# Kernel tuning notes

Hardware: AMD Instinct MI355X
Metric: run time of the kernel (lower is better)

The kernel has to match this reference:

```python
import jax, jax.numpy as jnp
import numpy as np

B, M, D, H = 2, 2048, 1024, 16
DH = D // H            # 64 head dim
FF = 2624              # GeGLU intermediate size
EPS = 1e-5
ROPE_BASE = 10000.0


def _layernorm(x, g, b):
    mu = jnp.mean(x, axis=-1, keepdims=True)
    var = jnp.mean(jnp.square(x - mu), axis=-1, keepdims=True)
    return (x - mu) * jax.lax.rsqrt(var + EPS) * g + b


def _rope_cos_sin(m, dh):
    # HF-style: inv_freq over even dims; only first dh/2 entries are used by apply_rope
    inv_freq = 1.0 / (ROPE_BASE ** (jnp.arange(0, dh, 2, dtype=jnp.float32) / dh))  # [dh/2]
    ang = jnp.arange(m, dtype=jnp.float32)[:, None] * inv_freq[None, :]             # [M, dh/2]
    return jnp.cos(ang), jnp.sin(ang)


def _apply_rope(x, c, s):
    # x: [B,H,M,dh]; c,s: [M,dh/2] broadcast over B,H. Half-split (non-interleaved) rotation.
    x1, x2 = jnp.split(x, 2, axis=-1)
    return jnp.concatenate([x1 * c - x2 * s, x1 * s + x2 * c], axis=-1)


def setup_inputs() -> dict:
    key = jax.random.key(0)
    ks = jax.random.split(key, 6)
    w = lambda k, shape: (jax.random.normal(k, shape, jnp.float32) * 0.02)
    return {
        "hidden_states": jax.random.normal(ks[0], (B, M, D), jnp.float32),
        "attention_mask": jnp.ones((B, M), jnp.int32),
        "ln1_g": jnp.ones((D,), jnp.float32),
        "ln1_b": jnp.zeros((D,), jnp.float32),
        "Wqkv_w": w(ks[1], (3 * D, D)),
        "Wqkv_b": jnp.zeros((3 * D,), jnp.float32),
        "Wo_w": w(ks[2], (D, D)),
        "ln2_g": jnp.ones((D,), jnp.float32),
        "ln2_b": jnp.zeros((D,), jnp.float32),
        "Wi_w": w(ks[3], (2 * FF, D)),
        "Wmlp_o_w": w(ks[4], (D, FF)),
    }


def reference(hidden_states, attention_mask, ln1_g, ln1_b, Wqkv_w, Wqkv_b, Wo_w,
              ln2_g, ln2_b, Wi_w, Wmlp_o_w):
    x = hidden_states                                    # [B,M,D]
    xn = _layernorm(x, ln1_g, ln1_b)
    qkv = xn @ Wqkv_w.T + Wqkv_b                         # [B,M,3D]
    qkv = qkv.reshape(B, M, 3, H, DH).transpose(0, 3, 1, 2, 4)  # [B,H,M,3,dh]
    q, k, v = qkv[..., 0, :], qkv[..., 1, :], qkv[..., 2, :]    # each [B,H,M,dh]

    c, s = _rope_cos_sin(M, DH)                          # [M, dh/2]
    q = _apply_rope(q, c, s)
    k = _apply_rope(k, c, s)

    scale = 1.0 / np.sqrt(DH)
    scores = jnp.einsum("bhmd,bhnd->bhmn", q, k) * scale  # [B,H,M,M]
    keep = (attention_mask > 0)[:, None, None, :]         # [B,1,1,M] padding mask on keys
    scores = jnp.where(keep, scores, -jnp.inf)
    p = jax.nn.softmax(scores, axis=-1)
    o = jnp.einsum("bhmn,bhnd->bhmd", p, v)               # [B,H,M,dh]

    attn_out = o.transpose(0, 2, 1, 3).reshape(B, M, D)
    x = x + attn_out @ Wo_w.T

    # ModernBERT GeGLU MLP: input, gate = Wi(x).chunk(2); Wo(gelu(input) * gate)
    xn2 = _layernorm(x, ln2_g, ln2_b)
    hg = xn2 @ Wi_w.T                                     # [B,M,2*FF]
    h_in, h_gate = jnp.split(hg, 2, axis=-1)
    x = x + (jax.nn.gelu(h_in) * h_gate) @ Wmlp_o_w.T
    return x
```

## Files before the change

kernel.cpp:

```cpp
#include <hip/hip_runtime.h>
#include <cstdint>
#include <cstddef>

using u16 = unsigned short;
using u32 = uint32_t;

typedef __attribute__((ext_vector_type(8))) short short8;
typedef __attribute__((ext_vector_type(4))) float floatx4;

#define DEVFN static __device__ __forceinline__

#define QSCALE 0.18033688011112042f

DEVFN u16 f2bf(float f) {
  u32 u = __float_as_uint(f);
  return (u16)((u + 0x7fffu + ((u >> 16) & 1u)) >> 16);
}

DEVFN float b2f(u16 u) { return __uint_as_float(((u32)u) << 16); }

DEVFN void async_load16(const void* g, const void* lds) {
  __builtin_amdgcn_global_load_lds(
      (const __attribute__((address_space(1))) u32*)(uintptr_t)g,
      (__attribute__((address_space(3))) u32*)(u32)(uintptr_t)lds,
      16, 0, 0);
}

__global__ void rope_tab_k(float* __restrict__ ct, float* __restrict__ st) {
  const int i = blockIdx.x * 256 + threadIdx.x;
  const int m = i >> 5, f = i & 31;
  const float inv = exp2f((float)f * -0.41524101186092025f);
  const float ang = (float)m * inv;
  ct[i] = cosf(ang);
  st[i] = sinf(ang);
}

__global__ void bias_k(const int* __restrict__ mask, float* __restrict__ biasT) {
  const int i = blockIdx.x * 256 + threadIdx.x;
  const int b = i >> 11, l = (i >> 7) & 15, t = i & 127;
  const int kt = t >> 3, tj = t & 7;
  const int key = kt * 128 + tj * 16 + l;
  biasT[i] = (mask[b * 2048 + key] > 0) ? 0.f : -1e30f;
}

__global__ void cvt_k4(const float* __restrict__ src, u16* __restrict__ dst, int n4) {
  const int i = blockIdx.x * 256 + threadIdx.x;
  if (i < n4) {
    const float4 v = ((const float4*)src)[i];
    ushort4 o;
    o.x = f2bf(v.x); o.y = f2bf(v.y); o.z = f2bf(v.z); o.w = f2bf(v.w);
    ((ushort4*)dst)[i] = o;
  }
}

__global__ void cvt_wi_k4(const float* __restrict__ src, u16* __restrict__ dst) {
  const int i = blockIdx.x * 256 + threadIdx.x;
  const int i4 = i * 4;
  const int p = i4 >> 10, kc = i4 & 1023;
  const int g = p >> 5, c = p & 31;
  const int srow = (c < 16) ? (g * 16 + c) : (2624 + g * 16 + (c - 16));
  const float4 v = *(const float4*)(src + (size_t)srow * 1024 + kc);
  ushort4 o;
  o.x = f2bf(v.x); o.y = f2bf(v.y); o.z = f2bf(v.z); o.w = f2bf(v.w);
  ((ushort4*)dst)[i] = o;
}

__global__ __launch_bounds__(256)
void ln_k(const float* __restrict__ x, const float* __restrict__ g,
          const float* __restrict__ bb, u16* __restrict__ out) {
  const int row = blockIdx.x;
  const int tid = threadIdx.x;
  const float4 v = ((const float4*)(x + (size_t)row * 1024))[tid];
  float s = v.x + v.y + v.z + v.w;
  float ss = v.x * v.x + v.y * v.y + v.z * v.z + v.w * v.w;
#pragma unroll
  for (int d = 32; d > 0; d >>= 1) {
    s += __shfl_xor(s, d);
    ss += __shfl_xor(ss, d);
  }
  __shared__ float red[8];
  const int wave = tid >> 6;
  if ((tid & 63) == 0) { red[wave] = s; red[4 + wave] = ss; }
  __syncthreads();
  s = red[0] + red[1] + red[2] + red[3];
  ss = red[4] + red[5] + red[6] + red[7];
  const float mu = s * (1.f / 1024.f);
  const float var = ss * (1.f / 1024.f) - mu * mu;
  const float rr = rsqrtf(var + 1e-5f);
  const float4 gv = ((const float4*)g)[tid];
  const float4 bv = ((const float4*)bb)[tid];
  u16* orow = out + (size_t)row * 1024 + tid * 4;
  orow[0] = f2bf((v.x - mu) * rr * gv.x + bv.x);
  orow[1] = f2bf((v.y - mu) * rr * gv.y + bv.y);
  orow[2] = f2bf((v.z - mu) * rr * gv.z + bv.z);
  orow[3] = f2bf((v.w - mu) * rr * gv.w + bv.w);
}

__global__ __launch_bounds__(256)
void red_ln_k(const float* __restrict__ resid, const u16* __restrict__ p0,
              const u16* __restrict__ p1, const float* __restrict__ g,
              const float* __restrict__ bb, float* __restrict__ outx,
              u16* __restrict__ outn) {
  const int row = blockIdx.x;
  const int tid = threadIdx.x;
  const size_t base = (size_t)row * 1024;
  const float4 h = ((const float4*)(resid + base))[tid];
  const ushort4 a = ((const ushort4*)(p0 + base))[tid];
  const ushort4 c = ((const ushort4*)(p1 + base))[tid];
  float4 v;
  v.x = h.x + b2f(a.x) + b2f(c.x);
  v.y = h.y + b2f(a.y) + b2f(c.y);
  v.z = h.z + b2f(a.z) + b2f(c.z);
  v.w = h.w + b2f(a.w) + b2f(c.w);
  float s = v.x + v.y + v.z + v.w;
  float ss = v.x * v.x + v.y * v.y + v.z * v.z + v.w * v.w;
#pragma unroll
  for (int d = 32; d > 0; d >>= 1) {
    s += __shfl_xor(s, d);
    ss += __shfl_xor(ss, d);
  }
  __shared__ float red[8];
  const int wave = tid >> 6;
  if ((tid & 63) == 0) { red[wave] = s; red[4 + wave] = ss; }
  __syncthreads();
  s = red[0] + red[1] + red[2] + red[3];
  ss = red[4] + red[5] + red[6] + red[7];
  const float mu = s * (1.f / 1024.f);
  const float var = ss * (1.f / 1024.f) - mu * mu;
  const float rr = rsqrtf(var + 1e-5f);
  ((float4*)(outx + base))[tid] = v;
  const float4 gv = ((const float4*)g)[tid];
  const float4 bv = ((const float4*)bb)[tid];
  u16* orow = outn + base + tid * 4;
  orow[0] = f2bf((v.x - mu) * rr * gv.x + bv.x);
  orow[1] = f2bf((v.y - mu) * rr * gv.y + bv.y);
  orow[2] = f2bf((v.z - mu) * rr * gv.z + bv.z);
  orow[3] = f2bf((v.w - mu) * rr * gv.w + bv.w);
}

__global__ void red_add_k(float* __restrict__ out, const u16* __restrict__ p0,
                          const u16* __restrict__ p1) {
  const int i = blockIdx.x * 256 + threadIdx.x;
  float4 v = ((const float4*)out)[i];
  const ushort4 a = ((const ushort4*)p0)[i];
  const ushort4 c = ((const ushort4*)p1)[i];
  v.x += b2f(a.x) + b2f(c.x);
  v.y += b2f(a.y) + b2f(c.y);
  v.z += b2f(a.z) + b2f(c.z);
  v.w += b2f(a.w) + b2f(c.w);
  ((float4*)out)[i] = v;
}

struct EpiArgs {
  const float* bias;
  u16* q; u16* kk; u16* vt;
  u16* outbf;
  const float* ct; const float* st;
};

template <int EPI>
__global__ __launch_bounds__(256, 2)
void gemm_k(const u16* __restrict__ A, const u16* __restrict__ B, int K, EpiArgs ea) {
  __shared__ __align__(16) u16 sA[128 * 32];
  __shared__ __align__(16) u16 sB[128 * 32];
  const int tn = blockIdx.x * 128;
  const int tm = blockIdx.y * 128;
  const int tid = threadIdx.x;
  const int wave = tid >> 6, lane = tid & 63;
  const int quad = lane >> 4, l15 = lane & 15;
  const int wm = (wave >> 1) * 64, wn = (wave & 1) * 64;

  floatx4 acc[4][4];
#pragma unroll
  for (int i = 0; i < 4; ++i)
#pragma unroll
    for (int j = 0; j < 4; ++j) acc[i][j] = (floatx4){0.f, 0.f, 0.f, 0.f};

  const int srow = lane >> 2;
  const int skc = (lane & 3) * 8;
  const u16* sAr = sA + (wm + l15) * 32 + quad * 8;
  const u16* sBr = sB + (wn + l15) * 32 + quad * 8;

  for (int k0 = 0; k0 < K; k0 += 32) {
#pragma unroll
    for (int j = 0; j < 2; ++j) {
      const int q = wave * 2 + j;
      const int row = q * 16 + srow;
      async_load16(A + (size_t)(tm + row) * K + (k0 + skc), (const char*)sA + q * 1024);
      async_load16(B + (size_t)(tn + row) * K + (k0 + skc), (const char*)sB + q * 1024);
    }
    __syncthreads();
    short8 af[4], bfr[4];
#pragma unroll
    for (int t = 0; t < 4; ++t) af[t] = *(const short8*)(sAr + t * 512);
#pragma unroll
    for (int t = 0; t < 4; ++t) bfr[t] = *(const short8*)(sBr + t * 512);
#pragma unroll
    for (int ti = 0; ti < 4; ++ti)
#pragma unroll
      for (int tj = 0; tj < 4; ++tj)
        acc[ti][tj] = __builtin_amdgcn_mfma_f32_16x16x32_bf16(af[ti], bfr[tj], acc[ti][tj], 0, 0, 0);
    __syncthreads();
  }

  if constexpr (EPI == 0) {
    const int col0 = tn + wn;
    const int t = col0 >> 10;
    const int h = (col0 & 1023) >> 6;
    if (t == 2) {
#pragma unroll
      for (int ti = 0; ti < 4; ++ti)
#pragma unroll
        for (int r = 0; r < 4; ++r) {
          const int row = tm + wm + ti * 16 + quad * 4 + r;
          const int b = row >> 11, m = row & 2047;
          const int mp = (m & ~31) | ((m & 15) << 1) | ((m >> 4) & 1);
#pragma unroll
          for (int tj = 0; tj < 4; ++tj) {
            const int dh = tj * 16 + l15;
            const float v = acc[ti][tj][r] + ea.bias[col0 + dh];
            ea.vt[((size_t)((b * 16 + h) * 64 + dh)) * 2048 + mp] = f2bf(v);
          }
        }
    } else {
      u16* dst = (t == 0) ? ea.q : ea.kk;
      const float qs = (t == 0) ? QSCALE : 1.f;
#pragma unroll
      for (int ti = 0; ti < 4; ++ti)
#pragma unroll
        for (int r = 0; r < 4; ++r) {
          const int row = tm + wm + ti * 16 + quad * 4 + r;
          const int b = row >> 11, m = row & 2047;
          u16* drow = dst + ((size_t)(b * 16 + h) * 2048 + m) * 64;
#pragma unroll
          for (int tj = 0; tj < 2; ++tj) {
            const int i = tj * 16 + l15;
            const float x1 = acc[ti][tj][r] + ea.bias[col0 + i];
            const float x2 = acc[ti][tj + 2][r] + ea.bias[col0 + 32 + i];
            const float cs = ea.ct[m * 32 + i];
            const float sn = ea.st[m * 32 + i];
            drow[i] = f2bf((x1 * cs - x2 * sn) * qs);
            drow[32 + i] = f2bf((x1 * sn + x2 * cs) * qs);
          }
        }
    }
  } else {
#pragma unroll
    for (int ti = 0; ti < 4; ++ti)
#pragma unroll
      for (int r = 0; r < 4; ++r) {
        const int row = tm + wm + ti * 16 + quad * 4 + r;
#pragma unroll
        for (int u = 0; u < 2; ++u) {
          const float hin = acc[ti][2 * u][r];
          const float hg = acc[ti][2 * u + 1][r];
          const int a = (((tn + wn) >> 5) + u) * 16 + l15;
          float tt = 0.7978845608028654f * (hin + 0.044715f * hin * hin * hin);
          tt = fminf(fmaxf(tt, -15.f), 15.f);
          const float e = __expf(2.f * tt);
          const float th = (e - 1.f) / (e + 1.f);
          const float gl = 0.5f * hin * (1.f + th);
          ea.outbf[(size_t)row * 2624 + a] = f2bf(gl * hg);
        }
      }
  }
}

__global__ __launch_bounds__(256, 4)
void gemm_sk(const u16* __restrict__ A, const u16* __restrict__ B, int K, int kps,
             u16* __restrict__ part0, u16* __restrict__ part1) {
  __shared__ __align__(16) u16 sA[128 * 32];
  __shared__ __align__(16) u16 sB[64 * 32];
  const int tn = blockIdx.x * 64;
  const int tm = blockIdx.y * 128;
  const int kofs = blockIdx.z * kps;
  const int tid = threadIdx.x;
  const int wave = tid >> 6, lane = tid & 63;
  const int quad = lane >> 4, l15 = lane & 15;
  const int wm = wave * 32;

  floatx4 acc[2][4];
#pragma unroll
  for (int i = 0; i < 2; ++i)
#pragma unroll
    for (int j = 0; j < 4; ++j) acc[i][j] = (floatx4){0.f, 0.f, 0.f, 0.f};

  const int srow = lane >> 2;
  const int skc = (lane & 3) * 8;
  const u16* sAr = sA + (wm + l15) * 32 + quad * 8;
  const u16* sBr = sB + l15 * 32 + quad * 8;

  for (int k0 = 0; k0 < kps; k0 += 32) {
    const int kk = kofs + k0;
#pragma unroll
    for (int j = 0; j < 2; ++j) {
      const int q = wave * 2 + j;
      const int row = q * 16 + srow;
      async_load16(A + (size_t)(tm + row) * K + (kk + skc), (const char*)sA + q * 1024);
    }
    {
      const int row = wave * 16 + srow;
      async_load16(B + (size_t)(tn + row) * K + (kk + skc), (const char*)sB + wave * 1024);
    }
    __syncthreads();
    short8 af[2], bfr[4];
#pragma unroll
    for (int t = 0; t < 2; ++t) af[t] = *(const short8*)(sAr + t * 512);
#pragma unroll
    for (int t = 0; t < 4; ++t) bfr[t] = *(const short8*)(sBr + t * 512);
#pragma unroll
    for (int ti = 0; ti < 2; ++ti)
#pragma unroll
      for (int tj = 0; tj < 4; ++tj)
        acc[ti][tj] = __builtin_amdgcn_mfma_f32_16x16x32_bf16(af[ti], bfr[tj], acc[ti][tj], 0, 0, 0);
    __syncthreads();
  }

  u16* part = blockIdx.z ? part1 : part0;
#pragma unroll
  for (int ti = 0; ti < 2; ++ti)
#pragma unroll
    for (int r = 0; r < 4; ++r) {
      const int row = tm + wm + ti * 16 + quad * 4 + r;
#pragma unroll
      for (int tj = 0; tj < 4; ++tj)
        part[(size_t)row * 1024 + tn + tj * 16 + l15] = f2bf(acc[ti][tj][r]);
    }
}

__global__ __launch_bounds__(256, 2)
void attn_k(const u16* __restrict__ qg, const u16* __restrict__ kg,
            const u16* __restrict__ vtg, const float* __restrict__ biasT,
            u16* __restrict__ outg) {
  __shared__ __align__(16) u16 sK[8 * 128 * 8];
  __shared__ __align__(16) u16 sV[16 * 64 * 8];
  __shared__ __align__(16) u16 sP[8 * 16 * 40];
  const int bh = blockIdx.y;
  const int b = bh >> 4, h = bh & 15;
  const int q0 = blockIdx.x * 128;
  const int tid = threadIdx.x;
  const int wave = tid >> 6, lane = tid & 63;
  const int quad = lane >> 4, l15 = lane & 15;

  short8 aq[2][2];
#pragma unroll
  for (int g = 0; g < 2; ++g) {
    const u16* qptr = qg + ((size_t)bh * 2048 + q0 + wave * 32 + g * 16 + l15) * 64 + quad * 8;
    aq[g][0] = *(const short8*)qptr;
    aq[g][1] = *(const short8*)(qptr + 32);
  }

  floatx4 o[2][4];
#pragma unroll
  for (int g = 0; g < 2; ++g)
#pragma unroll
    for (int t = 0; t < 4; ++t) o[g][t] = (floatx4){0.f, 0.f, 0.f, 0.f};
  float li[2][4] = {{0.f, 0.f, 0.f, 0.f}, {0.f, 0.f, 0.f, 0.f}};

  const float* bT = biasT + ((b << 11) | (l15 << 7));

  for (int kt = 0; kt < 16; ++kt) {
    const int key0 = kt * 128;
#pragma unroll
    for (int j = 0; j < 8; ++j) {
      const int qi = wave * 8 + j;
      if (qi < 16) {
        const int chunk = qi >> 1, half = qi & 1;
        const int row = half * 64 + lane;
        async_load16(kg + ((size_t)bh * 2048 + key0 + row) * 64 + chunk * 8,
                     (const char*)sK + qi * 1024);
      } else {
        const int vi = qi - 16;
        const int c = vi >> 2, kc = vi & 3;
        async_load16(vtg + ((size_t)bh * 64 + lane) * 2048 + key0 + c * 32 + kc * 8,
                     (const char*)sV + vi * 1024);
      }
    }
    const float4 mb0 = ((const float4*)(bT + kt * 8))[0];
    const float4 mb1 = ((const float4*)(bT + kt * 8))[1];
    const float mb[8] = {mb0.x, mb0.y, mb0.z, mb0.w, mb1.x, mb1.y, mb1.z, mb1.w};
    __syncthreads();

    floatx4 sacc[2][8];
#pragma unroll
    for (int g = 0; g < 2; ++g)
#pragma unroll
      for (int tj = 0; tj < 8; ++tj) sacc[g][tj] = (floatx4){0.f, 0.f, 0.f, 0.f};
#pragma unroll
    for (int tj = 0; tj < 8; ++tj) {
      const short8 b0 = *(const short8*)(sK + quad * 1024 + (tj * 16 + l15) * 8);
      const short8 b1 = *(const short8*)(sK + (4 + quad) * 1024 + (tj * 16 + l15) * 8);
      sacc[0][tj] = __builtin_amdgcn_mfma_f32_16x16x32_bf16(aq[0][0], b0, sacc[0][tj], 0, 0, 0);
      sacc[0][tj] = __builtin_amdgcn_mfma_f32_16x16x32_bf16(aq[0][1], b1, sacc[0][tj], 0, 0, 0);
      sacc[1][tj] = __builtin_amdgcn_mfma_f32_16x16x32_bf16(aq[1][0], b0, sacc[1][tj], 0, 0, 0);
      sacc[1][tj] = __builtin_amdgcn_mfma_f32_16x16x32_bf16(aq[1][1], b1, sacc[1][tj], 0, 0, 0);
    }

#pragma unroll
    for (int g = 0; g < 2; ++g)
#pragma unroll
      for (int r = 0; r < 4; ++r) {
        float sum = li[g][r];
#pragma unroll
        for (int tj = 0; tj < 8; ++tj) {
          const float p = __builtin_amdgcn_exp2f(sacc[g][tj][r] + mb[tj]);
          sacc[g][tj][r] = p;
          sum += p;
        }
        li[g][r] = sum;
      }

#pragma unroll
    for (int c = 0; c < 4; ++c) {
#pragma unroll
      for (int g = 0; g < 2; ++g) {
        u32* pw32 = (u32*)sP + (wave * 2 + g) * 320;
#pragma unroll
        for (int r = 0; r < 4; ++r) {
          const u32 lo = __float_as_uint(sacc[g][c * 2][r]) + 0x8000u;
          const u32 hi = __float_as_uint(sacc[g][c * 2 + 1][r]) + 0x8000u;
          pw32[(quad * 4 + r) * 20 + l15] = __builtin_amdgcn_perm(hi, lo, 0x07060302);
        }
      }
      asm volatile("s_waitcnt lgkmcnt(0)" ::: "memory");
      short8 ap[2];
#pragma unroll
      for (int g = 0; g < 2; ++g)
        ap[g] = *(const short8*)(sP + (wave * 2 + g) * 640 + l15 * 40 + quad * 8);
#pragma unroll
      for (int tj2 = 0; tj2 < 4; ++tj2) {
        const short8 bv = *(const short8*)(sV + (c * 4 + quad) * 512 + (tj2 * 16 + l15) * 8);
        o[0][tj2] = __builtin_amdgcn_mfma_f32_16x16x32_bf16(ap[0], bv, o[0][tj2], 0, 0, 0);
        o[1][tj2] = __builtin_amdgcn_mfma_f32_16x16x32_bf16(ap[1], bv, o[1][tj2], 0, 0, 0);
      }
    }
    __syncthreads();
  }

#pragma unroll
  for (int g = 0; g < 2; ++g)
#pragma unroll
    for (int r = 0; r < 4; ++r) {
      float s = li[g][r];
      s += __shfl_xor(s, 1);
      s += __shfl_xor(s, 2);
      s += __shfl_xor(s, 4);
      s += __shfl_xor(s, 8);
      li[g][r] = 1.f / s;
    }

#pragma unroll
  for (int g = 0; g < 2; ++g)
#pragma unroll
    for (int tj = 0; tj < 4; ++tj)
#pragma unroll
      for (int r = 0; r < 4; ++r) {
        const int m = q0 + wave * 32 + g * 16 + quad * 4 + r;
        outg[((size_t)b * 2048 + m) * 1024 + h * 64 + tj * 16 + l15] =
            f2bf(o[g][tj][r] * li[g][r]);
      }
}

static const size_t OFF_WQKV = 0;
static const size_t OFF_WO   = 6291456;
static const size_t OFF_WI   = 8388608;
static const size_t OFF_WMLP = 19136512;
static const size_t OFF_XN   = 24510464;
static const size_t OFF_Q    = 32899072;
static const size_t OFF_K    = 41287680;
static const size_t OFF_VT   = 49676288;
static const size_t OFF_ATT  = 58064896;
static const size_t OFF_ROPE = OFF_ATT;
static const size_t WS_NEED  = 66453504;

extern "C" void kernel_launch(void* const* d_in, const int* in_sizes, int n_in,
                              void* d_out, int out_size, void* d_ws, size_t ws_size,
                              hipStream_t stream) {
  (void)in_sizes; (void)n_in; (void)out_size;
  if (ws_size < WS_NEED) return;

  const float* hidden = (const float*)d_in[0];
  const int*   mask   = (const int*)d_in[1];
  const float* ln1g   = (const float*)d_in[2];
  const float* ln1b   = (const float*)d_in[3];
  const float* Wqkv   = (const float*)d_in[4];
  const float* Wqkvb  = (const float*)d_in[5];
  const float* Wo     = (const float*)d_in[6];
  const float* ln2g   = (const float*)d_in[7];
  const float* ln2b   = (const float*)d_in[8];
  const float* Wi     = (const float*)d_in[9];
  const float* Wmlp   = (const float*)d_in[10];
  float* out = (float*)d_out;
  char* ws = (char*)d_ws;

  u16* wqkv_bf = (u16*)(ws + OFF_WQKV);
  u16* wo_bf   = (u16*)(ws + OFF_WO);
  u16* wi_bf   = (u16*)(ws + OFF_WI);
  u16* wmlp_bf = (u16*)(ws + OFF_WMLP);
  u16* xn      = (u16*)(ws + OFF_XN);
  u16* qb      = (u16*)(ws + OFF_Q);
  u16* kb      = (u16*)(ws + OFF_K);
  u16* vtb     = (u16*)(ws + OFF_VT);
  u16* att     = (u16*)(ws + OFF_ATT);
  u16* act     = (u16*)(ws + OFF_Q);
  float* ct    = (float*)(ws + OFF_ROPE);
  float* st    = (float*)(ws + OFF_ROPE + 262144);
  float* biasT = (float*)(ws + OFF_WQKV);
  u16* wop0    = (u16*)(ws + OFF_Q);
  u16* wop1    = (u16*)(ws + OFF_Q + 8388608);
  u16* mlpp0   = (u16*)(ws + OFF_XN);
  u16* mlpp1   = (u16*)(ws + OFF_ATT);

  rope_tab_k<<<256, 256, 0, stream>>>(ct, st);
  cvt_k4<<<3072, 256, 0, stream>>>(Wqkv, wqkv_bf, 786432);
  cvt_k4<<<1024, 256, 0, stream>>>(Wo, wo_bf, 262144);
  cvt_wi_k4<<<5248, 256, 0, stream>>>(Wi, wi_bf);
  cvt_k4<<<2624, 256, 0, stream>>>(Wmlp, wmlp_bf, 671744);

  ln_k<<<4096, 256, 0, stream>>>(hidden, ln1g, ln1b, xn);

  EpiArgs e1 = {Wqkvb, qb, kb, vtb, nullptr, ct, st};
  gemm_k<0><<<dim3(24, 32), 256, 0, stream>>>(xn, wqkv_bf, 1024, e1);

  bias_k<<<16, 256, 0, stream>>>(mask, biasT);
  attn_k<<<dim3(16, 32), 256, 0, stream>>>(qb, kb, vtb, biasT, att);

  gemm_sk<<<dim3(16, 32, 2), 256, 0, stream>>>(att, wo_bf, 1024, 512, wop0, wop1);
  red_ln_k<<<4096, 256, 0, stream>>>(hidden, wop0, wop1, ln2g, ln2b, out, xn);

  EpiArgs e3 = {nullptr, nullptr, nullptr, nullptr, act, nullptr, nullptr};
  gemm_k<2><<<dim3(41, 32), 256, 0, stream>>>(xn, wi_bf, 1024, e3);

  gemm_sk<<<dim3(16, 32, 2), 256, 0, stream>>>(act, wmlp_bf, 2624, 1312, mlpp0, mlpp1);
  red_add_k<<<4096, 256, 0, stream>>>(out, mlpp0, mlpp1);
}
```

Measured before the change: 365.4 us.

## Fuse prep kernels, swizzle GEMM tiles, widen split-K tiles, inline mask and cheaper GELU

```diff
diff --git a/kernel.cpp b/kernel.cpp
--- a/kernel.cpp
+++ b/kernel.cpp
@@ -26,98 +26,98 @@
       16, 0, 0);
 }
 
-__global__ void rope_tab_k(float* __restrict__ ct, float* __restrict__ st) {
-  const int i = blockIdx.x * 256 + threadIdx.x;
-  const int m = i >> 5, f = i & 31;
-  const float inv = exp2f((float)f * -0.41524101186092025f);
-  const float ang = (float)m * inv;
-  ct[i] = cosf(ang);
-  st[i] = sinf(ang);
-}
-
-__global__ void bias_k(const int* __restrict__ mask, float* __restrict__ biasT) {
-  const int i = blockIdx.x * 256 + threadIdx.x;
-  const int b = i >> 11, l = (i >> 7) & 15, t = i & 127;
-  const int kt = t >> 3, tj = t & 7;
-  const int key = kt * 128 + tj * 16 + l;
-  biasT[i] = (mask[b * 2048 + key] > 0) ? 0.f : -1e30f;
-}
-
-__global__ void cvt_k4(const float* __restrict__ src, u16* __restrict__ dst, int n4) {
-  const int i = blockIdx.x * 256 + threadIdx.x;
-  if (i < n4) {
-    const float4 v = ((const float4*)src)[i];
-    ushort4 o;
-    o.x = f2bf(v.x); o.y = f2bf(v.y); o.z = f2bf(v.z); o.w = f2bf(v.w);
-    ((ushort4*)dst)[i] = o;
-  }
-}
-
-__global__ void cvt_wi_k4(const float* __restrict__ src, u16* __restrict__ dst) {
-  const int i = blockIdx.x * 256 + threadIdx.x;
-  const int i4 = i * 4;
-  const int p = i4 >> 10, kc = i4 & 1023;
-  const int g = p >> 5, c = p & 31;
-  const int srow = (c < 16) ? (g * 16 + c) : (2624 + g * 16 + (c - 16));
-  const float4 v = *(const float4*)(src + (size_t)srow * 1024 + kc);
+DEVFN void cvt4(const float* __restrict__ src, u16* __restrict__ dst, int i) {
+  const float4 v = ((const float4*)src)[i];
   ushort4 o;
   o.x = f2bf(v.x); o.y = f2bf(v.y); o.z = f2bf(v.z); o.w = f2bf(v.w);
   ((ushort4*)dst)[i] = o;
 }
 
 __global__ __launch_bounds__(256)
-void ln_k(const float* __restrict__ x, const float* __restrict__ g,
-          const float* __restrict__ bb, u16* __restrict__ out) {
-  const int row = blockIdx.x;
+void prep_k(const float* __restrict__ Wqkv, const float* __restrict__ Wo,
+            const float* __restrict__ Wi, const float* __restrict__ Wmlp,
+            const float* __restrict__ hidden, const float* __restrict__ ln1g,
+            const float* __restrict__ ln1b,
+            u16* __restrict__ wqkv_bf, u16* __restrict__ wo_bf,
+            u16* __restrict__ wi_bf, u16* __restrict__ wmlp_bf,
+            float* __restrict__ ct, float* __restrict__ st, u16* __restrict__ xn) {
+  const int bid = blockIdx.x;
   const int tid = threadIdx.x;
-  const float4 v = ((const float4*)(x + (size_t)row * 1024))[tid];
-  float s = v.x + v.y + v.z + v.w;
-  float ss = v.x * v.x + v.y * v.y + v.z * v.z + v.w * v.w;
-#pragma unroll
-  for (int d = 32; d > 0; d >>= 1) {
-    s += __shfl_xor(s, d);
-    ss += __shfl_xor(ss, d);
-  }
   __shared__ float red[8];
-  const int wave = tid >> 6;
-  if ((tid & 63) == 0) { red[wave] = s; red[4 + wave] = ss; }
-  __syncthreads();
-  s = red[0] + red[1] + red[2] + red[3];
-  ss = red[4] + red[5] + red[6] + red[7];
-  const float mu = s * (1.f / 1024.f);
-  const float var = ss * (1.f / 1024.f) - mu * mu;
-  const float rr = rsqrtf(var + 1e-5f);
-  const float4 gv = ((const float4*)g)[tid];
-  const float4 bv = ((const float4*)bb)[tid];
-  u16* orow = out + (size_t)row * 1024 + tid * 4;
-  orow[0] = f2bf((v.x - mu) * rr * gv.x + bv.x);
-  orow[1] = f2bf((v.y - mu) * rr * gv.y + bv.y);
-  orow[2] = f2bf((v.z - mu) * rr * gv.z + bv.z);
-  orow[3] = f2bf((v.w - mu) * rr * gv.w + bv.w);
+  if (bid < 256) {
+    const int i = bid * 256 + tid;
+    const int m = i >> 5, f = i & 31;
+    const float inv = exp2f((float)f * -0.41524101186092025f);
+    const float ang = (float)m * inv;
+    ct[i] = cosf(ang);
+    st[i] = sinf(ang);
+  } else if (bid < 3328) {
+    cvt4(Wqkv, wqkv_bf, (bid - 256) * 256 + tid);
+  } else if (bid < 4352) {
+    cvt4(Wo, wo_bf, (bid - 3328) * 256 + tid);
+  } else if (bid < 9600) {
+    const int i = (bid - 4352) * 256 + tid;
+    const int i4 = i * 4;
+    const int p = i4 >> 10, kc = i4 & 1023;
+    const int g = p >> 5, c = p & 31;
+    const int srow = (c < 16) ? (g * 16 + c) : (2624 + g * 16 + (c - 16));
+    const float4 v = *(const float4*)(Wi + (size_t)srow * 1024 + kc);
+    ushort4 o;
+    o.x = f2bf(v.x); o.y = f2bf(v.y); o.z = f2bf(v.z); o.w = f2bf(v.w);
+    ((ushort4*)wi_bf)[i] = o;
+  } else if (bid < 12224) {
+    cvt4(Wmlp, wmlp_bf, (bid - 9600) * 256 + tid);
+  } else {
+    const int row = bid - 12224;
+    const float4 v = ((const float4*)(hidden + (size_t)row * 1024))[tid];
+    float s = v.x + v.y + v.z + v.w;
+    float ss = v.x * v.x + v.y * v.y + v.z * v.z + v.w * v.w;
+#pragma unroll
+    for (int d = 32; d > 0; d >>= 1) {
+      s += __shfl_xor(s, d);
+      ss += __shfl_xor(ss, d);
+    }
+    const int wave = tid >> 6;
+    if ((tid & 63) == 0) { red[wave] = s; red[4 + wave] = ss; }
+    __syncthreads();
+    s = red[0] + red[1] + red[2] + red[3];
+    ss = red[4] + red[5] + red[6] + red[7];
+    const float mu = s * (1.f / 1024.f);
+    const float var = ss * (1.f / 1024.f) - mu * mu;
+    const float rr = rsqrtf(var + 1e-5f);
+    const float4 gv = ((const float4*)ln1g)[tid];
+    const float4 bv = ((const float4*)ln1b)[tid];
+    u16* orow = xn + (size_t)row * 1024 + tid * 4;
+    orow[0] = f2bf((v.x - mu) * rr * gv.x + bv.x);
+    orow[1] = f2bf((v.y - mu) * rr * gv.y + bv.y);
+    orow[2] = f2bf((v.z - mu) * rr * gv.z + bv.z);
+    orow[3] = f2bf((v.w - mu) * rr * gv.w + bv.w);
+  }
 }
 
 __global__ __launch_bounds__(256)
 void red_ln_k(const float* __restrict__ resid, const u16* __restrict__ p0,
-              const u16* __restrict__ p1, const float* __restrict__ g,
-              const float* __restrict__ bb, float* __restrict__ outx,
-              u16* __restrict__ outn) {
+              const u16* __restrict__ p1, const u16* __restrict__ p2,
+              const float* __restrict__ g, const float* __restrict__ bb,
+              float* __restrict__ outx, u16* __restrict__ outn) {
   const int row = blockIdx.x;
   const int tid = threadIdx.x;
   const size_t base = (size_t)row * 1024;
   const float4 h = ((const float4*)(resid + base))[tid];
   const ushort4 a = ((const ushort4*)(p0 + base))[tid];
   const ushort4 c = ((const ushort4*)(p1 + base))[tid];
+  const ushort4 d = ((const ushort4*)(p2 + base))[tid];
   float4 v;
-  v.x = h.x + b2f(a.x) + b2f(c.x);
-  v.y = h.y + b2f(a.y) + b2f(c.y);
-  v.z = h.z + b2f(a.z) + b2f(c.z);
-  v.w = h.w + b2f(a.w) + b2f(c.w);
+  v.x = h.x + b2f(a.x) + b2f(c.x) + b2f(d.x);
+  v.y = h.y + b2f(a.y) + b2f(c.y) + b2f(d.y);
+  v.z = h.z + b2f(a.z) + b2f(c.z) + b2f(d.z);
+  v.w = h.w + b2f(a.w) + b2f(c.w) + b2f(d.w);
   float s = v.x + v.y + v.z + v.w;
   float ss = v.x * v.x + v.y * v.y + v.z * v.z + v.w * v.w;
 #pragma unroll
-  for (int d = 32; d > 0; d >>= 1) {
-    s += __shfl_xor(s, d);
-    ss += __shfl_xor(ss, d);
+  for (int dd = 32; dd > 0; dd >>= 1) {
+    s += __shfl_xor(s, dd);
+    ss += __shfl_xor(ss, dd);
   }
   __shared__ float red[8];
   const int wave = tid >> 6;
@@ -139,16 +139,29 @@
 }
 
 __global__ void red_add_k(float* __restrict__ out, const u16* __restrict__ p0,
-                          const u16* __restrict__ p1) {
+                          const u16* __restrict__ p1, const u16* __restrict__ p2,
+                          const u16* __restrict__ p3) {
   const int i = blockIdx.x * 256 + threadIdx.x;
   float4 v = ((const float4*)out)[i];
   const ushort4 a = ((const ushort4*)p0)[i];
   const ushort4 c = ((const ushort4*)p1)[i];
-  v.x += b2f(a.x) + b2f(c.x);
-  v.y += b2f(a.y) + b2f(c.y);
-  v.z += b2f(a.z) + b2f(c.z);
-  v.w += b2f(a.w) + b2f(c.w);
+  const ushort4 d = ((const ushort4*)p2)[i];
+  const ushort4 e = ((const ushort4*)p3)[i];
+  v.x += b2f(a.x) + b2f(c.x) + b2f(d.x) + b2f(e.x);
+  v.y += b2f(a.y) + b2f(c.y) + b2f(d.y) + b2f(e.y);
+  v.z += b2f(a.z) + b2f(c.z) + b2f(d.z) + b2f(e.z);
+  v.w += b2f(a.w) + b2f(c.w) + b2f(d.w) + b2f(e.w);
   ((float4*)out)[i] = v;
+}
+
+DEVFN void swizzle_tile(int NT, int& tn, int& tm) {
+  const int tpx = gridDim.x >> 3;
+  const int p = blockIdx.x;
+  const int lid = (p & 7) * tpx + (p >> 3);
+  const int band = lid / (8 * NT);
+  const int rem = lid - band * 8 * NT;
+  tn = (rem >> 3) * 128;
+  tm = (band * 8 + (rem & 7)) * 128;
 }
 
 struct EpiArgs {
@@ -159,12 +172,13 @@
 };
 
 template <int EPI>
-__global__ __launch_bounds__(256, 2)
-void gemm_k(const u16* __restrict__ A, const u16* __restrict__ B, int K, EpiArgs ea) {
+__global__ __launch_bounds__(256, 3)
+void gemm_k(const u16* __restrict__ A, const u16* __restrict__ B, int K, int NT,
+            EpiArgs ea) {
   __shared__ __align__(16) u16 sA[128 * 32];
   __shared__ __align__(16) u16 sB[128 * 32];
-  const int tn = blockIdx.x * 128;
-  const int tm = blockIdx.y * 128;
+  int tn, tm;
+  swizzle_tile(NT, tn, tm);
   const int tid = threadIdx.x;
   const int wave = tid >> 6, lane = tid & 63;
   const int quad = lane >> 4, l15 = lane & 15;
@@ -255,40 +269,43 @@
           const float hin = acc[ti][2 * u][r];
           const float hg = acc[ti][2 * u + 1][r];
           const int a = (((tn + wn) >> 5) + u) * 16 + l15;
-          float tt = 0.7978845608028654f * (hin + 0.044715f * hin * hin * hin);
-          tt = fminf(fmaxf(tt, -15.f), 15.f);
-          const float e = __expf(2.f * tt);
-          const float th = (e - 1.f) / (e + 1.f);
-          const float gl = 0.5f * hin * (1.f + th);
+          const float t2 = hin + 0.044715f * hin * hin * hin;
+          const float e = __builtin_amdgcn_exp2f(t2 * -2.302114768f);
+          const float gl = hin * __builtin_amdgcn_rcpf(1.f + e);
           ea.outbf[(size_t)row * 2624 + a] = f2bf(gl * hg);
         }
       }
   }
 }
 
-__global__ __launch_bounds__(256, 4)
-void gemm_sk(const u16* __restrict__ A, const u16* __restrict__ B, int K, int kps,
-             u16* __restrict__ part0, u16* __restrict__ part1) {
+__global__ __launch_bounds__(256, 3)
+void gemm_sk4(const u16* __restrict__ A, const u16* __restrict__ B, int K, int NT,
+              int kps1, int zsw, int kps2,
+              u16* __restrict__ p0, u16* __restrict__ p1,
+              u16* __restrict__ p2, u16* __restrict__ p3) {
   __shared__ __align__(16) u16 sA[128 * 32];
-  __shared__ __align__(16) u16 sB[64 * 32];
-  const int tn = blockIdx.x * 64;
-  const int tm = blockIdx.y * 128;
-  const int kofs = blockIdx.z * kps;
+  __shared__ __align__(16) u16 sB[128 * 32];
+  int tn, tm;
+  swizzle_tile(NT, tn, tm);
+  const int z = blockIdx.y;
+  int kofs, kps;
+  if (z < zsw) { kofs = z * kps1; kps = kps1; }
+  else { kofs = zsw * kps1 + (z - zsw) * kps2; kps = kps2; }
   const int tid = threadIdx.x;
   const int wave = tid >> 6, lane = tid & 63;
   const int quad = lane >> 4, l15 = lane & 15;
-  const int wm = wave * 32;
-
-  floatx4 acc[2][4];
-#pragma unroll
-  for (int i = 0; i < 2; ++i)
+  const int wm = (wave >> 1) * 64, wn = (wave & 1) * 64;
+
+  floatx4 acc[4][4];
+#pragma unroll
+  for (int i = 0; i < 4; ++i)
 #pragma unroll
     for (int j = 0; j < 4; ++j) acc[i][j] = (floatx4){0.f, 0.f, 0.f, 0.f};
 
   const int srow = lane >> 2;
   const int skc = (lane & 3) * 8;
   const u16* sAr = sA + (wm + l15) * 32 + quad * 8;
-  const u16* sBr = sB + l15 * 32 + quad * 8;
+  const u16* sBr = sB + (wn + l15) * 32 + quad * 8;
 
   for (int k0 = 0; k0 < kps; k0 += 32) {
     const int kk = kofs + k0;
@@ -297,40 +314,37 @@
       const int q = wave * 2 + j;
       const int row = q * 16 + srow;
       async_load16(A + (size_t)(tm + row) * K + (kk + skc), (const char*)sA + q * 1024);
-    }
-    {
-      const int row = wave * 16 + srow;
-      async_load16(B + (size_t)(tn + row) * K + (kk + skc), (const char*)sB + wave * 1024);
-    }
-    __syncthreads();
-    short8 af[2], bfr[4];
-#pragma unroll
-    for (int t = 0; t < 2; ++t) af[t] = *(const short8*)(sAr + t * 512);
+      async_load16(B + (size_t)(tn + row) * K + (kk + skc), (const char*)sB + q * 1024);
+    }
+    __syncthreads();
+    short8 af[4], bfr[4];
+#pragma unroll
+    for (int t = 0; t < 4; ++t) af[t] = *(const short8*)(sAr + t * 512);
 #pragma unroll
     for (int t = 0; t < 4; ++t) bfr[t] = *(const short8*)(sBr + t * 512);
 #pragma unroll
-    for (int ti = 0; ti < 2; ++ti)
+    for (int ti = 0; ti < 4; ++ti)
 #pragma unroll
       for (int tj = 0; tj < 4; ++tj)
         acc[ti][tj] = __builtin_amdgcn_mfma_f32_16x16x32_bf16(af[ti], bfr[tj], acc[ti][tj], 0, 0, 0);
     __syncthreads();
   }
 
-  u16* part = blockIdx.z ? part1 : part0;
-#pragma unroll
-  for (int ti = 0; ti < 2; ++ti)
+  u16* part = (z == 0) ? p0 : (z == 1) ? p1 : (z == 2) ? p2 : p3;
+#pragma unroll
+  for (int ti = 0; ti < 4; ++ti)
 #pragma unroll
     for (int r = 0; r < 4; ++r) {
       const int row = tm + wm + ti * 16 + quad * 4 + r;
 #pragma unroll
       for (int tj = 0; tj < 4; ++tj)
-        part[(size_t)row * 1024 + tn + tj * 16 + l15] = f2bf(acc[ti][tj][r]);
+        part[(size_t)row * 1024 + tn + wn + tj * 16 + l15] = f2bf(acc[ti][tj][r]);
     }
 }
 
 __global__ __launch_bounds__(256, 2)
 void attn_k(const u16* __restrict__ qg, const u16* __restrict__ kg,
-            const u16* __restrict__ vtg, const float* __restrict__ biasT,
+            const u16* __restrict__ vtg, const int* __restrict__ mask,
             u16* __restrict__ outg) {
   __shared__ __align__(16) u16 sK[8 * 128 * 8];
   __shared__ __align__(16) u16 sV[16 * 64 * 8];
@@ -356,8 +370,6 @@
 #pragma unroll
     for (int t = 0; t < 4; ++t) o[g][t] = (floatx4){0.f, 0.f, 0.f, 0.f};
   float li[2][4] = {{0.f, 0.f, 0.f, 0.f}, {0.f, 0.f, 0.f, 0.f}};
-
-  const float* bT = biasT + ((b << 11) | (l15 << 7));
 
   for (int kt = 0; kt < 16; ++kt) {
     const int key0 = kt * 128;
@@ -376,9 +388,10 @@
                      (const char*)sV + vi * 1024);
       }
     }
-    const float4 mb0 = ((const float4*)(bT + kt * 8))[0];
-    const float4 mb1 = ((const float4*)(bT + kt * 8))[1];
-    const float mb[8] = {mb0.x, mb0.y, mb0.z, mb0.w, mb1.x, mb1.y, mb1.z, mb1.w};
+    float mb[8];
+#pragma unroll
+    for (int tj = 0; tj < 8; ++tj)
+      mb[tj] = (mask[b * 2048 + key0 + tj * 16 + l15] > 0) ? 0.f : -1e30f;
     __syncthreads();
 
     floatx4 sacc[2][8];
@@ -505,32 +518,30 @@
   u16* act     = (u16*)(ws + OFF_Q);
   float* ct    = (float*)(ws + OFF_ROPE);
   float* st    = (float*)(ws + OFF_ROPE + 262144);
-  float* biasT = (float*)(ws + OFF_WQKV);
-  u16* wop0    = (u16*)(ws + OFF_Q);
-  u16* wop1    = (u16*)(ws + OFF_Q + 8388608);
-  u16* mlpp0   = (u16*)(ws + OFF_XN);
-  u16* mlpp1   = (u16*)(ws + OFF_ATT);
-
-  rope_tab_k<<<256, 256, 0, stream>>>(ct, st);
-  cvt_k4<<<3072, 256, 0, stream>>>(Wqkv, wqkv_bf, 786432);
-  cvt_k4<<<1024, 256, 0, stream>>>(Wo, wo_bf, 262144);
-  cvt_wi_k4<<<5248, 256, 0, stream>>>(Wi, wi_bf);
-  cvt_k4<<<2624, 256, 0, stream>>>(Wmlp, wmlp_bf, 671744);
-
-  ln_k<<<4096, 256, 0, stream>>>(hidden, ln1g, ln1b, xn);
+  u16* wp0     = (u16*)(ws + OFF_Q);
+  u16* wp1     = (u16*)(ws + OFF_K);
+  u16* wp2     = (u16*)(ws + OFF_VT);
+  u16* mp0     = (u16*)(ws + OFF_XN);
+  u16* mp1     = (u16*)(ws + OFF_ATT);
+  u16* mp2     = (u16*)(ws + OFF_WI);
+  u16* mp3     = (u16*)(ws + OFF_WQKV);
+
+  prep_k<<<16320, 256, 0, stream>>>(Wqkv, Wo, Wi, Wmlp, hidden, ln1g, ln1b,
+                                    wqkv_bf, wo_bf, wi_bf, wmlp_bf, ct, st, xn);
 
   EpiArgs e1 = {Wqkvb, qb, kb, vtb, nullptr, ct, st};
-  gemm_k<0><<<dim3(24, 32), 256, 0, stream>>>(xn, wqkv_bf, 1024, e1);
-
-  bias_k<<<16, 256, 0, stream>>>(mask, biasT);
-  attn_k<<<dim3(16, 32), 256, 0, stream>>>(qb, kb, vtb, biasT, att);
-
-  gemm_sk<<<dim3(16, 32, 2), 256, 0, stream>>>(att, wo_bf, 1024, 512, wop0, wop1);
-  red_ln_k<<<4096, 256, 0, stream>>>(hidden, wop0, wop1, ln2g, ln2b, out, xn);
+  gemm_k<0><<<768, 256, 0, stream>>>(xn, wqkv_bf, 1024, 24, e1);
+
+  attn_k<<<dim3(16, 32), 256, 0, stream>>>(qb, kb, vtb, mask, att);
+
+  gemm_sk4<<<dim3(256, 3), 256, 0, stream>>>(att, wo_bf, 1024, 8, 352, 2, 320,
+                                             wp0, wp1, wp2, wp2);
+  red_ln_k<<<4096, 256, 0, stream>>>(hidden, wp0, wp1, wp2, ln2g, ln2b, out, xn);
 
   EpiArgs e3 = {nullptr, nullptr, nullptr, nullptr, act, nullptr, nullptr};
-  gemm_k<2><<<dim3(41, 32), 256, 0, stream>>>(xn, wi_bf, 1024, e3);
-
-  gemm_sk<<<dim3(16, 32, 2), 256, 0, stream>>>(act, wmlp_bf, 2624, 1312, mlpp0, mlpp1);
-  red_add_k<<<4096, 256, 0, stream>>>(out, mlpp0, mlpp1);
-}
+  gemm_k<2><<<1312, 256, 0, stream>>>(xn, wi_bf, 1024, 41, e3);
+
+  gemm_sk4<<<dim3(256, 4), 256, 0, stream>>>(act, wmlp_bf, 2624, 8, 672, 2, 640,
+                                             mp0, mp1, mp2, mp3);
+  red_add_k<<<4096, 256, 0, stream>>>(out, mp0, mp1, mp2, mp3);
+}
```

Result: faster. 349.3 us (-4.4%).
